# Kernel tuning notes

Measured on AMD Instinct MI355X. Metric: run time of the kernel, lower is better.

Reference implementation:

```python
import jax, jax.numpy as jnp
import numpy as np

B, H, O, M = 8192, 1024, 1024, 4

def setup_inputs() -> dict:
    key = jax.random.key(0)
    ks = jax.random.split(key, 8)
    state = jax.random.normal(ks[0], (B, H), dtype=jnp.float32)
    spectral_entropy = jax.random.uniform(ks[1], (B, 1), dtype=jnp.float32)
    curvature = jax.random.normal(ks[2], (B, 1), dtype=jnp.float32)
    # learned params
    modulation_basis = jax.random.normal(ks[3], (M, H, O), dtype=jnp.float32)
    gate_w = jax.random.normal(ks[4], (1, M), dtype=jnp.float32) / jnp.sqrt(1.0)
    gate_b = jax.random.normal(ks[5], (M,), dtype=jnp.float32) * 0.01
    prj_w = jax.random.normal(ks[6], (H, O), dtype=jnp.float32) / jnp.sqrt(H)
    prj_b = jax.random.normal(ks[7], (O,), dtype=jnp.float32) * 0.01
    return {"state": state, "spectral_entropy": spectral_entropy, "curvature": curvature,
            "modulation_basis": modulation_basis, "gate_w": gate_w, "gate_b": gate_b,
            "prj_w": prj_w, "prj_b": prj_b}

def reference(state, spectral_entropy, curvature, modulation_basis, gate_w, gate_b, prj_w, prj_b):
    # softmax gate over modes: [B, M]
    mod_weights = jax.nn.softmax(spectral_entropy @ gate_w + gate_b, axis=-1)
    # Algebraically fused form of einsum('bm,mho->bho') then einsum('bh,bho->bo'):
    # compute per-mode matvec results [B, M, O] (small), then mode-weighted sum.
    mode_out = jnp.einsum('bh,mho->bmo', state, modulation_basis)
    mischief_output = jnp.einsum('bm,bmo->bo', mod_weights, mode_out)
    base_output = state @ prj_w + prj_b
    mix = jax.nn.sigmoid(curvature)  # [B, 1]
    return (1.0 - mix) * base_output + mix * mischief_output
```

## Files before the change

kernel.cpp:

```cpp
#include <hip/hip_runtime.h>
#include <stdint.h>

typedef __attribute__((ext_vector_type(4))) float  float4v;
typedef __attribute__((ext_vector_type(8))) __bf16 bf16x8;
typedef __attribute__((ext_vector_type(8))) unsigned short ushort8;

#define B_DIM 8192
#define H_DIM 1024
#define O_DIM 1024

static __device__ __forceinline__ unsigned short f32_to_bf16(float f) {
  union { float f; unsigned int u; } v; v.f = f;
  unsigned int u = v.u;
  unsigned int r = u + 0x7FFFu + ((u >> 16) & 1u);
  return (unsigned short)(r >> 16);
}

__global__ void prep_inputs(const float* __restrict__ state,
                            const float* __restrict__ basis,
                            const float* __restrict__ prjw,
                            unsigned short* __restrict__ Abf,
                            unsigned short* __restrict__ Wt) {
  __shared__ __align__(16) unsigned short t[64 * 72];
  int bb = blockIdx.x;
  int tid = threadIdx.x;
  if (bb < 1280) {
    int m = bb >> 8, panel = bb & 255;
    int o0 = (panel & 15) * 64, h0 = (panel >> 4) * 64;
    const float* src = (m < 4) ? (basis + (size_t)m * H_DIM * O_DIM) : prjw;
    int r  = tid >> 4;
    int c4 = (tid & 15) * 4;
#pragma unroll
    for (int p = 0; p < 4; ++p) {
      int h = r + p * 16;
      float4v v = *(const float4v*)(src + (size_t)(h0 + h) * O_DIM + o0 + c4);
      t[(c4 + 0) * 72 + h] = f32_to_bf16(v.x);
      t[(c4 + 1) * 72 + h] = f32_to_bf16(v.y);
      t[(c4 + 2) * 72 + h] = f32_to_bf16(v.z);
      t[(c4 + 3) * 72 + h] = f32_to_bf16(v.w);
    }
    __syncthreads();
#pragma unroll
    for (int i = 0; i < 2; ++i) {
      int C = i * 256 + tid;
      int o = C >> 3, cc = C & 7;
      ushort8 val = *(const ushort8*)(t + o * 72 + cc * 8);
      *(ushort8*)(Wt + ((size_t)m * O_DIM + o0 + o) * H_DIM + h0 + cc * 8) = val;
    }
  } else {
    int i = (bb - 1280) * 256 + tid;
    float4v v0 = ((const float4v*)state)[i * 2];
    float4v v1 = ((const float4v*)state)[i * 2 + 1];
    ushort8 o;
    o[0] = f32_to_bf16(v0.x); o[1] = f32_to_bf16(v0.y);
    o[2] = f32_to_bf16(v0.z); o[3] = f32_to_bf16(v0.w);
    o[4] = f32_to_bf16(v1.x); o[5] = f32_to_bf16(v1.y);
    o[6] = f32_to_bf16(v1.z); o[7] = f32_to_bf16(v1.w);
    ((ushort8*)Abf)[i] = o;
  }
}

__global__ __launch_bounds__(512, 2)
void gemm_fused(const unsigned short* __restrict__ A,
                const unsigned short* __restrict__ Wt,
                const float* __restrict__ se, const float* __restrict__ curv,
                const float* __restrict__ gw, const float* __restrict__ gb,
                const float* __restrict__ prjb,
                float* __restrict__ out) {
  __shared__ __align__(16) unsigned char smem[115712];
  float* scf = (float*)(smem + 110592);

  const int tid  = threadIdx.x;
  const int lane = tid & 63;
  const int wave = tid >> 6;
  const int row0 = blockIdx.x * 256;
  const int col0 = blockIdx.y * 64;
  const int wrow = (wave >> 1) * 64;
  const int wcol = (wave & 1) * 32;
  const int q  = lane >> 4;
  const int ln = lane & 15;

  if (tid < 256) {
    int b = row0 + tid;
    float s = se[b];
    float l0 = fmaf(s, gw[0], gb[0]);
    float l1 = fmaf(s, gw[1], gb[1]);
    float l2 = fmaf(s, gw[2], gb[2]);
    float l3 = fmaf(s, gw[3], gb[3]);
    float mx = fmaxf(fmaxf(l0, l1), fmaxf(l2, l3));
    float e0 = __expf(l0 - mx), e1 = __expf(l1 - mx);
    float e2 = __expf(l2 - mx), e3 = __expf(l3 - mx);
    float mix = 1.0f / (1.0f + __expf(-curv[b]));
    float inv = mix / (e0 + e1 + e2 + e3);
    scf[0 * 256 + tid] = e0 * inv;
    scf[1 * 256 + tid] = e1 * inv;
    scf[2 * 256 + tid] = e2 * inv;
    scf[3 * 256 + tid] = e3 * inv;
    scf[4 * 256 + tid] = 1.0f - mix;
  }

  const unsigned short* gsrc[5];
  unsigned int ldsoff[5];
  if (wave < 4) {
#pragma unroll
    for (int j = 0; j < 4; ++j) {
      int c = wave * 4 + j;
      int row = c * 16 + (lane >> 2);
      int pos = lane & 3;
      int g = pos ^ ((row >> 1) & 3);
      gsrc[j] = A + (size_t)(row0 + row) * H_DIM + g * 8;
      ldsoff[j] = c * 1024;
    }
    gsrc[4] = gsrc[0]; ldsoff[4] = ldsoff[0];
  } else {
#pragma unroll
    for (int j = 0; j < 5; ++j) {
      int c = (wave - 4) * 5 + j;
      int m = c >> 2;
      int r = (c & 3) * 16 + (lane >> 2);
      int pos = lane & 3;
      int g = pos ^ ((r >> 1) & 3);
      gsrc[j] = Wt + (size_t)m * O_DIM * H_DIM + (size_t)(col0 + r) * H_DIM + g * 8;
      ldsoff[j] = 16384 + c * 1024;
    }
  }

  float4v acc[5][4][2];
#pragma unroll
  for (int m = 0; m < 5; ++m)
#pragma unroll
    for (int i = 0; i < 4; ++i)
#pragma unroll
      for (int j = 0; j < 2; ++j)
        acc[m][i][j] = (float4v){0.f, 0.f, 0.f, 0.f};

#define ISSUE_STAGE(koff, boff)                                                 \
  do {                                                                          \
    if (wave < 4) {                                                             \
      _Pragma("unroll")                                                         \
      for (int _j = 0; _j < 4; ++_j)                                            \
        __builtin_amdgcn_global_load_lds(                                       \
            (const __attribute__((address_space(1))) void*)(gsrc[_j] + (koff)), \
            (__attribute__((address_space(3))) void*)(smem + (boff) + ldsoff[_j]),\
            16, 0, 0);                                                          \
    } else {                                                                    \
      _Pragma("unroll")                                                         \
      for (int _j = 0; _j < 5; ++_j)                                            \
        __builtin_amdgcn_global_load_lds(                                       \
            (const __attribute__((address_space(1))) void*)(gsrc[_j] + (koff)), \
            (__attribute__((address_space(3))) void*)(smem + (boff) + ldsoff[_j]),\
            16, 0, 0);                                                          \
    }                                                                           \
  } while (0)

#define WAITV_STEADY                                                            \
  do {                                                                          \
    if (wave < 4) asm volatile("s_waitcnt vmcnt(8)" ::: "memory");              \
    else          asm volatile("s_waitcnt vmcnt(10)" ::: "memory");             \
  } while (0)
#define WAITV_ONE                                                               \
  do {                                                                          \
    if (wave < 4) asm volatile("s_waitcnt vmcnt(4)" ::: "memory");              \
    else          asm volatile("s_waitcnt vmcnt(5)" ::: "memory");              \
  } while (0)
#define WAITV_ZERO asm volatile("s_waitcnt vmcnt(0)" ::: "memory")

#define COMPUTE_STAGE(boff)                                                     \
  do {                                                                          \
    const unsigned short* _sA = (const unsigned short*)(smem + (boff));         \
    const unsigned short* _sB = _sA + 8192;                                     \
    __builtin_amdgcn_s_setprio(1);                                              \
    bf16x8 _af[4];                                                              \
    _Pragma("unroll")                                                           \
    for (int _t = 0; _t < 4; ++_t) {                                            \
      int _ra = wrow + _t * 16 + ln;                                            \
      int _ps = q ^ ((_ra >> 1) & 3);                                           \
      _af[_t] = *(const bf16x8*)(_sA + _ra * 32 + _ps * 8);                     \
    }                                                                           \
    _Pragma("unroll")                                                           \
    for (int _m = 0; _m < 5; ++_m) {                                            \
      bf16x8 _b0, _b1;                                                          \
      {                                                                         \
        int _rb = wcol + ln;                                                    \
        int _p0 = q ^ ((_rb >> 1) & 3);                                         \
        _b0 = *(const bf16x8*)(_sB + _m * 2048 + _rb * 32 + _p0 * 8);           \
        int _r1 = wcol + 16 + ln;                                               \
        int _p1 = q ^ ((_r1 >> 1) & 3);                                         \
        _b1 = *(const bf16x8*)(_sB + _m * 2048 + _r1 * 32 + _p1 * 8);           \
      }                                                                         \
      _Pragma("unroll")                                                         \
      for (int _ti = 0; _ti < 4; ++_ti) {                                       \
        acc[_m][_ti][0] = __builtin_amdgcn_mfma_f32_16x16x32_bf16(              \
            _af[_ti], _b0, acc[_m][_ti][0], 0, 0, 0);                           \
        acc[_m][_ti][1] = __builtin_amdgcn_mfma_f32_16x16x32_bf16(              \
            _af[_ti], _b1, acc[_m][_ti][1], 0, 0, 0);                           \
      }                                                                         \
    }                                                                           \
    __builtin_amdgcn_s_setprio(0);                                              \
  } while (0)

  ISSUE_STAGE(0, 0u);
  ISSUE_STAGE(32, 36864u);
  ISSUE_STAGE(64, 73728u);
  asm volatile("s_waitcnt lgkmcnt(0)" ::: "memory");
  WAITV_STEADY;
  __builtin_amdgcn_s_barrier();

  unsigned int boff = 0u;
  int kk = 96;
  for (int s = 0; s < 29; ++s) {
    COMPUTE_STAGE(boff);
    __builtin_amdgcn_s_barrier();
    ISSUE_STAGE(kk, boff);
    WAITV_STEADY;
    __builtin_amdgcn_s_barrier();
    kk += 32;
    boff = (boff == 73728u) ? 0u : boff + 36864u;
  }
  COMPUTE_STAGE(boff);
  WAITV_ONE;
  __builtin_amdgcn_s_barrier();
  boff = (boff == 73728u) ? 0u : boff + 36864u;
  COMPUTE_STAGE(boff);
  WAITV_ZERO;
  __builtin_amdgcn_s_barrier();
  boff = (boff == 73728u) ? 0u : boff + 36864u;
  COMPUTE_STAGE(boff);

  __syncthreads();
  float* fbuf = (float*)smem;
#pragma unroll
  for (int ti = 0; ti < 4; ++ti) {
    int rl = wrow + ti * 16 + q * 4;
#pragma unroll
    for (int tj = 0; tj < 2; ++tj) {
      int cc = wcol + tj * 16 + ln;
#pragma unroll
      for (int r = 0; r < 4; ++r) {
        float v = 0.f;
#pragma unroll
        for (int m = 0; m < 5; ++m)
          v += scf[m * 256 + rl + r] * acc[m][ti][tj][r];
        fbuf[(rl + r) * 68 + cc] = v;
      }
    }
  }
  __syncthreads();
#pragma unroll
  for (int i = 0; i < 8; ++i) {
    int L = i * 512 + tid;
    int row = L >> 4, c4 = L & 15;
    float4v v = *(const float4v*)(fbuf + row * 68 + c4 * 4);
    float cb = scf[4 * 256 + row];
    float4v pb = *(const float4v*)(prjb + col0 + c4 * 4);
    v += cb * pb;
    *(float4v*)(out + (size_t)(row0 + row) * O_DIM + col0 + c4 * 4) = v;
  }
#undef ISSUE_STAGE
#undef WAITV_STEADY
#undef WAITV_ONE
#undef WAITV_ZERO
#undef COMPUTE_STAGE
}

extern "C" void kernel_launch(void* const* d_in, const int* in_sizes, int n_in,
                              void* d_out, int out_size, void* d_ws, size_t ws_size,
                              hipStream_t stream) {
  const float* state = (const float*)d_in[0];
  const float* se    = (const float*)d_in[1];
  const float* curv  = (const float*)d_in[2];
  const float* basis = (const float*)d_in[3];
  const float* gw    = (const float*)d_in[4];
  const float* gb    = (const float*)d_in[5];
  const float* prjw  = (const float*)d_in[6];
  const float* prjb  = (const float*)d_in[7];
  float* out = (float*)d_out;

  char* ws = (char*)d_ws;
  unsigned short* Abf = (unsigned short*)ws;
  unsigned short* Wt  = (unsigned short*)(ws + (size_t)16 * 1024 * 1024);

  prep_inputs<<<5376, 256, 0, stream>>>(state, basis, prjw, Abf, Wt);
  dim3 gg(B_DIM / 256, O_DIM / 64);
  gemm_fused<<<gg, 512, 0, stream>>>(Abf, Wt, se, curv, gw, gb, prjb, out);
}
```

Before: 180.6 us.

## Switch to four-slot LDS ring with loads interleaved into per-mode MFMA phases

Grows the LDS staging ring from three to four slots, so the next global-to-LDS copy can target a free slot while the current one is still being read. That copy is now split across the first three mode phases of each K step, each phase bracketed by barriers and a raised-priority MFMA burst. It also precomputes the swizzled LDS fragment offsets and advances the global pointers incrementally. The aim is to hide memory latency behind MFMA work and drop the separate issue and barrier step that followed each compute stage. The cost is many more workgroup barriers per K step and a larger LDS footprint.

```diff
diff --git a/kernel.cpp b/kernel.cpp
--- a/kernel.cpp
+++ b/kernel.cpp
@@ -67,8 +67,8 @@
                 const float* __restrict__ gw, const float* __restrict__ gb,
                 const float* __restrict__ prjb,
                 float* __restrict__ out) {
-  __shared__ __align__(16) unsigned char smem[115712];
-  float* scf = (float*)(smem + 110592);
+  __shared__ __align__(16) unsigned char smem[152576];
+  float* scf = (float*)(smem + 147456);
 
   const int tid  = threadIdx.x;
   const int lane = tid & 63;
@@ -80,6 +80,140 @@
   const int q  = lane >> 4;
   const int ln = lane & 15;
 
+  const unsigned short* gsrc[5];
+  unsigned int ldsoff[5];
+  if (wave < 4) {
+#pragma unroll
+    for (int j = 0; j < 4; ++j) {
+      int c = wave * 4 + j;
+      int row = c * 16 + (lane >> 2);
+      int pos = lane & 3;
+      int g = pos ^ ((row >> 1) & 3);
+      gsrc[j] = A + (size_t)(row0 + row) * H_DIM + g * 8;
+      ldsoff[j] = c * 1024;
+    }
+    gsrc[4] = gsrc[0]; ldsoff[4] = ldsoff[0];
+  } else {
+#pragma unroll
+    for (int j = 0; j < 5; ++j) {
+      int c = (wave - 4) * 5 + j;
+      int m = c >> 2;
+      int r = (c & 3) * 16 + (lane >> 2);
+      int pos = lane & 3;
+      int g = pos ^ ((r >> 1) & 3);
+      gsrc[j] = Wt + (size_t)m * O_DIM * H_DIM + (size_t)(col0 + r) * H_DIM + g * 8;
+      ldsoff[j] = 16384 + c * 1024;
+    }
+  }
+
+  int aoffs[4];
+#pragma unroll
+  for (int t = 0; t < 4; ++t) {
+    int ra = wrow + t * 16 + ln;
+    aoffs[t] = ra * 32 + (q ^ ((ra >> 1) & 3)) * 8;
+  }
+  int boffs[2];
+  {
+    int rb = wcol + ln;      boffs[0] = rb * 32 + (q ^ ((rb >> 1) & 3)) * 8;
+    int r1 = wcol + 16 + ln; boffs[1] = r1 * 32 + (q ^ ((r1 >> 1) & 3)) * 8;
+  }
+
+  float4v acc[5][4][2];
+#pragma unroll
+  for (int m = 0; m < 5; ++m)
+#pragma unroll
+    for (int i = 0; i < 4; ++i)
+#pragma unroll
+      for (int j = 0; j < 2; ++j)
+        acc[m][i][j] = (float4v){0.f, 0.f, 0.f, 0.f};
+
+#define GLDS(j_)                                                                \
+  __builtin_amdgcn_global_load_lds(                                             \
+      (const __attribute__((address_space(1))) void*)(gsrc[j_]),                \
+      (__attribute__((address_space(3))) void*)(dst + ldsoff[j_]), 16, 0, 0)
+
+#define ISSUE_HALF(slot)                                                        \
+  do {                                                                          \
+    unsigned char* dst = smem + (slot) * 36864;                                 \
+    GLDS(0); GLDS(1); GLDS(2); GLDS(3);                                         \
+    if (wave >= 4) GLDS(4);                                                     \
+    _Pragma("unroll") for (int _j = 0; _j < 5; ++_j) gsrc[_j] += 32;            \
+  } while (0)
+
+#define GUARD_2L                                                                \
+  do { if (wave < 4) asm volatile("s_waitcnt vmcnt(8)" ::: "memory");           \
+       else          asm volatile("s_waitcnt vmcnt(10)" ::: "memory"); } while (0)
+#define GUARD_1L                                                                \
+  do { if (wave < 4) asm volatile("s_waitcnt vmcnt(4)" ::: "memory");           \
+       else          asm volatile("s_waitcnt vmcnt(5)" ::: "memory"); } while (0)
+#define GUARD_0   asm volatile("s_waitcnt vmcnt(0)" ::: "memory")
+#define GUARD_NONE do { } while (0)
+
+#define MFMA8(m_)                                                               \
+  do {                                                                          \
+    acc[m_][0][0] = __builtin_amdgcn_mfma_f32_16x16x32_bf16(af0, b0, acc[m_][0][0], 0, 0, 0); \
+    acc[m_][1][0] = __builtin_amdgcn_mfma_f32_16x16x32_bf16(af1, b0, acc[m_][1][0], 0, 0, 0); \
+    acc[m_][2][0] = __builtin_amdgcn_mfma_f32_16x16x32_bf16(af2, b0, acc[m_][2][0], 0, 0, 0); \
+    acc[m_][3][0] = __builtin_amdgcn_mfma_f32_16x16x32_bf16(af3, b0, acc[m_][3][0], 0, 0, 0); \
+    acc[m_][0][1] = __builtin_amdgcn_mfma_f32_16x16x32_bf16(af0, b1, acc[m_][0][1], 0, 0, 0); \
+    acc[m_][1][1] = __builtin_amdgcn_mfma_f32_16x16x32_bf16(af1, b1, acc[m_][1][1], 0, 0, 0); \
+    acc[m_][2][1] = __builtin_amdgcn_mfma_f32_16x16x32_bf16(af2, b1, acc[m_][2][1], 0, 0, 0); \
+    acc[m_][3][1] = __builtin_amdgcn_mfma_f32_16x16x32_bf16(af3, b1, acc[m_][3][1], 0, 0, 0); \
+  } while (0)
+
+#define PH_BAR_MFMA(m_)                                                         \
+  do {                                                                          \
+    __builtin_amdgcn_s_barrier();                                               \
+    asm volatile("s_waitcnt lgkmcnt(0)" ::: "memory");                          \
+    __builtin_amdgcn_s_setprio(1);                                              \
+    MFMA8(m_);                                                                  \
+    __builtin_amdgcn_s_setprio(0);                                              \
+  } while (0)
+
+#define HALF_TILE(hh, DO_GLDS, GUARD)                                           \
+  do {                                                                          \
+    const unsigned short* sA = (const unsigned short*)(smem + ((hh) & 3) * 36864);\
+    const unsigned short* sB = sA + 8192;                                       \
+    unsigned char* dst = smem + (((hh) + 3) & 3) * 36864; (void)dst;            \
+                                        \
+    bf16x8 af0 = *(const bf16x8*)(sA + aoffs[0]);                               \
+    bf16x8 af1 = *(const bf16x8*)(sA + aoffs[1]);                               \
+    bf16x8 af2 = *(const bf16x8*)(sA + aoffs[2]);                               \
+    bf16x8 af3 = *(const bf16x8*)(sA + aoffs[3]);                               \
+    bf16x8 b0 = *(const bf16x8*)(sB + boffs[0]);                                \
+    bf16x8 b1 = *(const bf16x8*)(sB + boffs[1]);                                \
+    if (DO_GLDS) { GLDS(0); GLDS(1); }                                          \
+    PH_BAR_MFMA(0);                                                             \
+    __builtin_amdgcn_s_barrier();                                               \
+                                                  \
+    b0 = *(const bf16x8*)(sB + 2048 + boffs[0]);                                \
+    b1 = *(const bf16x8*)(sB + 2048 + boffs[1]);                                \
+    if (DO_GLDS) { GLDS(2); GLDS(3); }                                          \
+    PH_BAR_MFMA(1);                                                             \
+    __builtin_amdgcn_s_barrier();                                               \
+                                \
+    b0 = *(const bf16x8*)(sB + 4096 + boffs[0]);                                \
+    b1 = *(const bf16x8*)(sB + 4096 + boffs[1]);                                \
+    if (DO_GLDS) {                                                              \
+      if (wave >= 4) GLDS(4);                                                   \
+      _Pragma("unroll") for (int _j = 0; _j < 5; ++_j) gsrc[_j] += 32;          \
+    }                                                                           \
+    PH_BAR_MFMA(2);                                                             \
+    __builtin_amdgcn_s_barrier();                                               \
+                                                          \
+    b0 = *(const bf16x8*)(sB + 6144 + boffs[0]);                                \
+    b1 = *(const bf16x8*)(sB + 6144 + boffs[1]);                                \
+    PH_BAR_MFMA(3);                                                             \
+    __builtin_amdgcn_s_barrier();                                               \
+                   \
+    b0 = *(const bf16x8*)(sB + 8192 + boffs[0]);                                \
+    b1 = *(const bf16x8*)(sB + 8192 + boffs[1]);                                \
+    PH_BAR_MFMA(4);                                                             \
+    GUARD;                                                                      \
+    __builtin_amdgcn_s_barrier();                                               \
+  } while (0)
+
+  ISSUE_HALF(0); ISSUE_HALF(1); ISSUE_HALF(2);
   if (tid < 256) {
     int b = row0 + tid;
     float s = se[b];
@@ -98,134 +232,20 @@
     scf[3 * 256 + tid] = e3 * inv;
     scf[4 * 256 + tid] = 1.0f - mix;
   }
-
-  const unsigned short* gsrc[5];
-  unsigned int ldsoff[5];
-  if (wave < 4) {
-#pragma unroll
-    for (int j = 0; j < 4; ++j) {
-      int c = wave * 4 + j;
-      int row = c * 16 + (lane >> 2);
-      int pos = lane & 3;
-      int g = pos ^ ((row >> 1) & 3);
-      gsrc[j] = A + (size_t)(row0 + row) * H_DIM + g * 8;
-      ldsoff[j] = c * 1024;
-    }
-    gsrc[4] = gsrc[0]; ldsoff[4] = ldsoff[0];
-  } else {
-#pragma unroll
-    for (int j = 0; j < 5; ++j) {
-      int c = (wave - 4) * 5 + j;
-      int m = c >> 2;
-      int r = (c & 3) * 16 + (lane >> 2);
-      int pos = lane & 3;
-      int g = pos ^ ((r >> 1) & 3);
-      gsrc[j] = Wt + (size_t)m * O_DIM * H_DIM + (size_t)(col0 + r) * H_DIM + g * 8;
-      ldsoff[j] = 16384 + c * 1024;
-    }
-  }
-
-  float4v acc[5][4][2];
-#pragma unroll
-  for (int m = 0; m < 5; ++m)
-#pragma unroll
-    for (int i = 0; i < 4; ++i)
-#pragma unroll
-      for (int j = 0; j < 2; ++j)
-        acc[m][i][j] = (float4v){0.f, 0.f, 0.f, 0.f};
-
-#define ISSUE_STAGE(koff, boff)                                                 \
-  do {                                                                          \
-    if (wave < 4) {                                                             \
-      _Pragma("unroll")                                                         \
-      for (int _j = 0; _j < 4; ++_j)                                            \
-        __builtin_amdgcn_global_load_lds(                                       \
-            (const __attribute__((address_space(1))) void*)(gsrc[_j] + (koff)), \
-            (__attribute__((address_space(3))) void*)(smem + (boff) + ldsoff[_j]),\
-            16, 0, 0);                                                          \
-    } else {                                                                    \
-      _Pragma("unroll")                                                         \
-      for (int _j = 0; _j < 5; ++_j)                                            \
-        __builtin_amdgcn_global_load_lds(                                       \
-            (const __attribute__((address_space(1))) void*)(gsrc[_j] + (koff)), \
-            (__attribute__((address_space(3))) void*)(smem + (boff) + ldsoff[_j]),\
-            16, 0, 0);                                                          \
-    }                                                                           \
-  } while (0)
-
-#define WAITV_STEADY                                                            \
-  do {                                                                          \
-    if (wave < 4) asm volatile("s_waitcnt vmcnt(8)" ::: "memory");              \
-    else          asm volatile("s_waitcnt vmcnt(10)" ::: "memory");             \
-  } while (0)
-#define WAITV_ONE                                                               \
-  do {                                                                          \
-    if (wave < 4) asm volatile("s_waitcnt vmcnt(4)" ::: "memory");              \
-    else          asm volatile("s_waitcnt vmcnt(5)" ::: "memory");              \
-  } while (0)
-#define WAITV_ZERO asm volatile("s_waitcnt vmcnt(0)" ::: "memory")
-
-#define COMPUTE_STAGE(boff)                                                     \
-  do {                                                                          \
-    const unsigned short* _sA = (const unsigned short*)(smem + (boff));         \
-    const unsigned short* _sB = _sA + 8192;                                     \
-    __builtin_amdgcn_s_setprio(1);                                              \
-    bf16x8 _af[4];                                                              \
-    _Pragma("unroll")                                                           \
-    for (int _t = 0; _t < 4; ++_t) {                                            \
-      int _ra = wrow + _t * 16 + ln;                                            \
-      int _ps = q ^ ((_ra >> 1) & 3);                                           \
-      _af[_t] = *(const bf16x8*)(_sA + _ra * 32 + _ps * 8);                     \
-    }                                                                           \
-    _Pragma("unroll")                                                           \
-    for (int _m = 0; _m < 5; ++_m) {                                            \
-      bf16x8 _b0, _b1;                                                          \
-      {                                                                         \
-        int _rb = wcol + ln;                                                    \
-        int _p0 = q ^ ((_rb >> 1) & 3);                                         \
-        _b0 = *(const bf16x8*)(_sB + _m * 2048 + _rb * 32 + _p0 * 8);           \
-        int _r1 = wcol + 16 + ln;                                               \
-        int _p1 = q ^ ((_r1 >> 1) & 3);                                         \
-        _b1 = *(const bf16x8*)(_sB + _m * 2048 + _r1 * 32 + _p1 * 8);           \
-      }                                                                         \
-      _Pragma("unroll")                                                         \
-      for (int _ti = 0; _ti < 4; ++_ti) {                                       \
-        acc[_m][_ti][0] = __builtin_amdgcn_mfma_f32_16x16x32_bf16(              \
-            _af[_ti], _b0, acc[_m][_ti][0], 0, 0, 0);                           \
-        acc[_m][_ti][1] = __builtin_amdgcn_mfma_f32_16x16x32_bf16(              \
-            _af[_ti], _b1, acc[_m][_ti][1], 0, 0, 0);                           \
-      }                                                                         \
-    }                                                                           \
-    __builtin_amdgcn_s_setprio(0);                                              \
-  } while (0)
-
-  ISSUE_STAGE(0, 0u);
-  ISSUE_STAGE(32, 36864u);
-  ISSUE_STAGE(64, 73728u);
   asm volatile("s_waitcnt lgkmcnt(0)" ::: "memory");
-  WAITV_STEADY;
+  GUARD_2L;
   __builtin_amdgcn_s_barrier();
 
-  unsigned int boff = 0u;
-  int kk = 96;
-  for (int s = 0; s < 29; ++s) {
-    COMPUTE_STAGE(boff);
-    __builtin_amdgcn_s_barrier();
-    ISSUE_STAGE(kk, boff);
-    WAITV_STEADY;
-    __builtin_amdgcn_s_barrier();
-    kk += 32;
-    boff = (boff == 73728u) ? 0u : boff + 36864u;
-  }
-  COMPUTE_STAGE(boff);
-  WAITV_ONE;
-  __builtin_amdgcn_s_barrier();
-  boff = (boff == 73728u) ? 0u : boff + 36864u;
-  COMPUTE_STAGE(boff);
-  WAITV_ZERO;
-  __builtin_amdgcn_s_barrier();
-  boff = (boff == 73728u) ? 0u : boff + 36864u;
-  COMPUTE_STAGE(boff);
+  for (int h = 0; h < 28; h += 4) {
+    HALF_TILE(h + 0, true, GUARD_2L);
+    HALF_TILE(h + 1, true, GUARD_2L);
+    HALF_TILE(h + 2, true, GUARD_2L);
+    HALF_TILE(h + 3, true, GUARD_2L);
+  }
+  HALF_TILE(28, true,  GUARD_2L);
+  HALF_TILE(29, false, GUARD_1L);
+  HALF_TILE(30, false, GUARD_0);
+  HALF_TILE(31, false, GUARD_NONE);
 
   __syncthreads();
   float* fbuf = (float*)smem;
@@ -256,11 +276,15 @@
     v += cb * pb;
     *(float4v*)(out + (size_t)(row0 + row) * O_DIM + col0 + c4 * 4) = v;
   }
-#undef ISSUE_STAGE
-#undef WAITV_STEADY
-#undef WAITV_ONE
-#undef WAITV_ZERO
-#undef COMPUTE_STAGE
+#undef GLDS
+#undef ISSUE_HALF
+#undef GUARD_2L
+#undef GUARD_1L
+#undef GUARD_0
+#undef GUARD_NONE
+#undef MFMA8
+#undef PH_BAR_MFMA
+#undef HALF_TILE
 }
 
 extern "C" void kernel_launch(void* const* d_in, const int* in_sizes, int n_in,
```

New measurement: 281.0 us. +55.6%, slower.

## Restructure GEMM main loop: one barrier per stage, prefetch fragments across barrier

Applied to the files above, without the earlier changes.

The K-loop is rewritten from two barriers per stage to a single barrier. The next stage's global-to-LDS copy is issued before computing, and the A and mode-0/1 B fragments for the following stage are read right after the barrier, so the LDS reads overlap the wait. Pointer increments and precomputed LDS offsets replace per-stage address math. Only two stages are prefetched before the gate softmax setup, which moves behind the first issues. This cuts synchronization and exposed LDS latency, at the cost of a shallower in-flight prefetch depth and more register pressure from the extra live fragments.

```diff
diff --git a/kernel.cpp b/kernel.cpp
--- a/kernel.cpp
+++ b/kernel.cpp
@@ -80,6 +80,129 @@
   const int q  = lane >> 4;
   const int ln = lane & 15;
 
+  const unsigned short* gsrc[5];
+  unsigned int ldsoff[5];
+  if (wave < 4) {
+#pragma unroll
+    for (int j = 0; j < 4; ++j) {
+      int c = wave * 4 + j;
+      int row = c * 16 + (lane >> 2);
+      int pos = lane & 3;
+      int g = pos ^ ((row >> 1) & 3);
+      gsrc[j] = A + (size_t)(row0 + row) * H_DIM + g * 8;
+      ldsoff[j] = c * 1024;
+    }
+    gsrc[4] = gsrc[0]; ldsoff[4] = ldsoff[0];
+  } else {
+#pragma unroll
+    for (int j = 0; j < 5; ++j) {
+      int c = (wave - 4) * 5 + j;
+      int m = c >> 2;
+      int r = (c & 3) * 16 + (lane >> 2);
+      int pos = lane & 3;
+      int g = pos ^ ((r >> 1) & 3);
+      gsrc[j] = Wt + (size_t)m * O_DIM * H_DIM + (size_t)(col0 + r) * H_DIM + g * 8;
+      ldsoff[j] = 16384 + c * 1024;
+    }
+  }
+
+  int aoffs[4];
+#pragma unroll
+  for (int t = 0; t < 4; ++t) {
+    int ra = wrow + t * 16 + ln;
+    aoffs[t] = ra * 32 + (q ^ ((ra >> 1) & 3)) * 8;
+  }
+  int boffs[2];
+  {
+    int rb = wcol + ln;      boffs[0] = rb * 32 + (q ^ ((rb >> 1) & 3)) * 8;
+    int r1 = wcol + 16 + ln; boffs[1] = r1 * 32 + (q ^ ((r1 >> 1) & 3)) * 8;
+  }
+
+  float4v acc[5][4][2];
+#pragma unroll
+  for (int m = 0; m < 5; ++m)
+#pragma unroll
+    for (int i = 0; i < 4; ++i)
+#pragma unroll
+      for (int j = 0; j < 2; ++j)
+        acc[m][i][j] = (float4v){0.f, 0.f, 0.f, 0.f};
+
+#define ISSUE_SLOT(boff_)                                                       \
+  do {                                                                          \
+    unsigned char* _dst = smem + (boff_);                                       \
+    __builtin_amdgcn_global_load_lds(                                           \
+        (const __attribute__((address_space(1))) void*)gsrc[0],                 \
+        (__attribute__((address_space(3))) void*)(_dst + ldsoff[0]), 16, 0, 0); \
+    __builtin_amdgcn_global_load_lds(                                           \
+        (const __attribute__((address_space(1))) void*)gsrc[1],                 \
+        (__attribute__((address_space(3))) void*)(_dst + ldsoff[1]), 16, 0, 0); \
+    __builtin_amdgcn_global_load_lds(                                           \
+        (const __attribute__((address_space(1))) void*)gsrc[2],                 \
+        (__attribute__((address_space(3))) void*)(_dst + ldsoff[2]), 16, 0, 0); \
+    __builtin_amdgcn_global_load_lds(                                           \
+        (const __attribute__((address_space(1))) void*)gsrc[3],                 \
+        (__attribute__((address_space(3))) void*)(_dst + ldsoff[3]), 16, 0, 0); \
+    if (wave >= 4)                                                              \
+      __builtin_amdgcn_global_load_lds(                                         \
+          (const __attribute__((address_space(1))) void*)gsrc[4],               \
+          (__attribute__((address_space(3))) void*)(_dst + ldsoff[4]), 16, 0, 0);\
+    _Pragma("unroll") for (int _j = 0; _j < 5; ++_j) gsrc[_j] += 32;            \
+  } while (0)
+
+#define WAITL                                                                   \
+  do { if (wave < 4) asm volatile("s_waitcnt vmcnt(4)" ::: "memory");           \
+       else          asm volatile("s_waitcnt vmcnt(5)" ::: "memory"); } while (0)
+
+  bf16x8 a0, a1, a2, a3, b00, b01, b10, b11;
+
+#define READ_PH0(boff_)                                                         \
+  do {                                                                          \
+    const unsigned short* _sA = (const unsigned short*)(smem + (boff_));        \
+    const unsigned short* _sB = _sA + 8192;                                     \
+    a0 = *(const bf16x8*)(_sA + aoffs[0]);                                      \
+    a1 = *(const bf16x8*)(_sA + aoffs[1]);                                      \
+    a2 = *(const bf16x8*)(_sA + aoffs[2]);                                      \
+    a3 = *(const bf16x8*)(_sA + aoffs[3]);                                      \
+    b00 = *(const bf16x8*)(_sB + boffs[0]);                                     \
+    b01 = *(const bf16x8*)(_sB + boffs[1]);                                     \
+    b10 = *(const bf16x8*)(_sB + 2048 + boffs[0]);                              \
+    b11 = *(const bf16x8*)(_sB + 2048 + boffs[1]);                              \
+  } while (0)
+
+#define MFMA_MODE(m_, bb0, bb1)                                                 \
+  do {                                                                          \
+    acc[m_][0][0] = __builtin_amdgcn_mfma_f32_16x16x32_bf16(a0, bb0, acc[m_][0][0], 0, 0, 0); \
+    acc[m_][1][0] = __builtin_amdgcn_mfma_f32_16x16x32_bf16(a1, bb0, acc[m_][1][0], 0, 0, 0); \
+    acc[m_][2][0] = __builtin_amdgcn_mfma_f32_16x16x32_bf16(a2, bb0, acc[m_][2][0], 0, 0, 0); \
+    acc[m_][3][0] = __builtin_amdgcn_mfma_f32_16x16x32_bf16(a3, bb0, acc[m_][3][0], 0, 0, 0); \
+    acc[m_][0][1] = __builtin_amdgcn_mfma_f32_16x16x32_bf16(a0, bb1, acc[m_][0][1], 0, 0, 0); \
+    acc[m_][1][1] = __builtin_amdgcn_mfma_f32_16x16x32_bf16(a1, bb1, acc[m_][1][1], 0, 0, 0); \
+    acc[m_][2][1] = __builtin_amdgcn_mfma_f32_16x16x32_bf16(a2, bb1, acc[m_][2][1], 0, 0, 0); \
+    acc[m_][3][1] = __builtin_amdgcn_mfma_f32_16x16x32_bf16(a3, bb1, acc[m_][3][1], 0, 0, 0); \
+  } while (0)
+
+#define PH1_READS(boff_)                                                        \
+  const unsigned short* _cB = (const unsigned short*)(smem + (boff_)) + 8192;   \
+  bf16x8 c20 = *(const bf16x8*)(_cB + 2 * 2048 + boffs[0]);                     \
+  bf16x8 c21 = *(const bf16x8*)(_cB + 2 * 2048 + boffs[1]);                     \
+  bf16x8 c30 = *(const bf16x8*)(_cB + 3 * 2048 + boffs[0]);                     \
+  bf16x8 c31 = *(const bf16x8*)(_cB + 3 * 2048 + boffs[1]);                     \
+  bf16x8 c40 = *(const bf16x8*)(_cB + 4 * 2048 + boffs[0]);                     \
+  bf16x8 c41 = *(const bf16x8*)(_cB + 4 * 2048 + boffs[1])
+
+#define MFMA_ALL5                                                               \
+  do {                                                                          \
+    __builtin_amdgcn_s_setprio(1);                                              \
+    MFMA_MODE(0, b00, b01);                                                     \
+    MFMA_MODE(1, b10, b11);                                                     \
+    MFMA_MODE(2, c20, c21);                                                     \
+    MFMA_MODE(3, c30, c31);                                                     \
+    MFMA_MODE(4, c40, c41);                                                     \
+    __builtin_amdgcn_s_setprio(0);                                              \
+  } while (0)
+
+  ISSUE_SLOT(0u);
+  ISSUE_SLOT(36864u);
   if (tid < 256) {
     int b = row0 + tid;
     float s = se[b];
@@ -98,134 +221,35 @@
     scf[3 * 256 + tid] = e3 * inv;
     scf[4 * 256 + tid] = 1.0f - mix;
   }
-
-  const unsigned short* gsrc[5];
-  unsigned int ldsoff[5];
-  if (wave < 4) {
-#pragma unroll
-    for (int j = 0; j < 4; ++j) {
-      int c = wave * 4 + j;
-      int row = c * 16 + (lane >> 2);
-      int pos = lane & 3;
-      int g = pos ^ ((row >> 1) & 3);
-      gsrc[j] = A + (size_t)(row0 + row) * H_DIM + g * 8;
-      ldsoff[j] = c * 1024;
-    }
-    gsrc[4] = gsrc[0]; ldsoff[4] = ldsoff[0];
-  } else {
-#pragma unroll
-    for (int j = 0; j < 5; ++j) {
-      int c = (wave - 4) * 5 + j;
-      int m = c >> 2;
-      int r = (c & 3) * 16 + (lane >> 2);
-      int pos = lane & 3;
-      int g = pos ^ ((r >> 1) & 3);
-      gsrc[j] = Wt + (size_t)m * O_DIM * H_DIM + (size_t)(col0 + r) * H_DIM + g * 8;
-      ldsoff[j] = 16384 + c * 1024;
-    }
-  }
-
-  float4v acc[5][4][2];
-#pragma unroll
-  for (int m = 0; m < 5; ++m)
-#pragma unroll
-    for (int i = 0; i < 4; ++i)
-#pragma unroll
-      for (int j = 0; j < 2; ++j)
-        acc[m][i][j] = (float4v){0.f, 0.f, 0.f, 0.f};
-
-#define ISSUE_STAGE(koff, boff)                                                 \
-  do {                                                                          \
-    if (wave < 4) {                                                             \
-      _Pragma("unroll")                                                         \
-      for (int _j = 0; _j < 4; ++_j)                                            \
-        __builtin_amdgcn_global_load_lds(                                       \
-            (const __attribute__((address_space(1))) void*)(gsrc[_j] + (koff)), \
-            (__attribute__((address_space(3))) void*)(smem + (boff) + ldsoff[_j]),\
-            16, 0, 0);                                                          \
-    } else {                                                                    \
-      _Pragma("unroll")                                                         \
-      for (int _j = 0; _j < 5; ++_j)                                            \
-        __builtin_amdgcn_global_load_lds(                                       \
-            (const __attribute__((address_space(1))) void*)(gsrc[_j] + (koff)), \
-            (__attribute__((address_space(3))) void*)(smem + (boff) + ldsoff[_j]),\
-            16, 0, 0);                                                          \
-    }                                                                           \
-  } while (0)
-
-#define WAITV_STEADY                                                            \
-  do {                                                                          \
-    if (wave < 4) asm volatile("s_waitcnt vmcnt(8)" ::: "memory");              \
-    else          asm volatile("s_waitcnt vmcnt(10)" ::: "memory");             \
-  } while (0)
-#define WAITV_ONE                                                               \
-  do {                                                                          \
-    if (wave < 4) asm volatile("s_waitcnt vmcnt(4)" ::: "memory");              \
-    else          asm volatile("s_waitcnt vmcnt(5)" ::: "memory");              \
-  } while (0)
-#define WAITV_ZERO asm volatile("s_waitcnt vmcnt(0)" ::: "memory")
-
-#define COMPUTE_STAGE(boff)                                                     \
-  do {                                                                          \
-    const unsigned short* _sA = (const unsigned short*)(smem + (boff));         \
-    const unsigned short* _sB = _sA + 8192;                                     \
-    __builtin_amdgcn_s_setprio(1);                                              \
-    bf16x8 _af[4];                                                              \
-    _Pragma("unroll")                                                           \
-    for (int _t = 0; _t < 4; ++_t) {                                            \
-      int _ra = wrow + _t * 16 + ln;                                            \
-      int _ps = q ^ ((_ra >> 1) & 3);                                           \
-      _af[_t] = *(const bf16x8*)(_sA + _ra * 32 + _ps * 8);                     \
-    }                                                                           \
-    _Pragma("unroll")                                                           \
-    for (int _m = 0; _m < 5; ++_m) {                                            \
-      bf16x8 _b0, _b1;                                                          \
-      {                                                                         \
-        int _rb = wcol + ln;                                                    \
-        int _p0 = q ^ ((_rb >> 1) & 3);                                         \
-        _b0 = *(const bf16x8*)(_sB + _m * 2048 + _rb * 32 + _p0 * 8);           \
-        int _r1 = wcol + 16 + ln;                                               \
-        int _p1 = q ^ ((_r1 >> 1) & 3);                                         \
-        _b1 = *(const bf16x8*)(_sB + _m * 2048 + _r1 * 32 + _p1 * 8);           \
-      }                                                                         \
-      _Pragma("unroll")                                                         \
-      for (int _ti = 0; _ti < 4; ++_ti) {                                       \
-        acc[_m][_ti][0] = __builtin_amdgcn_mfma_f32_16x16x32_bf16(              \
-            _af[_ti], _b0, acc[_m][_ti][0], 0, 0, 0);                           \
-        acc[_m][_ti][1] = __builtin_amdgcn_mfma_f32_16x16x32_bf16(              \
-            _af[_ti], _b1, acc[_m][_ti][1], 0, 0, 0);                           \
-      }                                                                         \
-    }                                                                           \
-    __builtin_amdgcn_s_setprio(0);                                              \
-  } while (0)
-
-  ISSUE_STAGE(0, 0u);
-  ISSUE_STAGE(32, 36864u);
-  ISSUE_STAGE(64, 73728u);
-  asm volatile("s_waitcnt lgkmcnt(0)" ::: "memory");
-  WAITV_STEADY;
+  WAITL;
   __builtin_amdgcn_s_barrier();
-
-  unsigned int boff = 0u;
-  int kk = 96;
-  for (int s = 0; s < 29; ++s) {
-    COMPUTE_STAGE(boff);
+  __builtin_amdgcn_sched_barrier(0);
+  READ_PH0(0u);
+
+  unsigned int cS = 0u, nS = 36864u, iS = 73728u;
+#pragma unroll 1
+  for (int s = 0; s < 30; ++s) {
+    ISSUE_SLOT(iS);
+    PH1_READS(cS);
+    MFMA_ALL5;
+    WAITL;
     __builtin_amdgcn_s_barrier();
-    ISSUE_STAGE(kk, boff);
-    WAITV_STEADY;
+    __builtin_amdgcn_sched_barrier(0);
+    READ_PH0(nS);
+    unsigned int t_ = cS; cS = nS; nS = iS; iS = t_;
+  }
+  {
+    PH1_READS(cS);
+    MFMA_ALL5;
+    asm volatile("s_waitcnt vmcnt(0)" ::: "memory");
     __builtin_amdgcn_s_barrier();
-    kk += 32;
-    boff = (boff == 73728u) ? 0u : boff + 36864u;
-  }
-  COMPUTE_STAGE(boff);
-  WAITV_ONE;
-  __builtin_amdgcn_s_barrier();
-  boff = (boff == 73728u) ? 0u : boff + 36864u;
-  COMPUTE_STAGE(boff);
-  WAITV_ZERO;
-  __builtin_amdgcn_s_barrier();
-  boff = (boff == 73728u) ? 0u : boff + 36864u;
-  COMPUTE_STAGE(boff);
+    __builtin_amdgcn_sched_barrier(0);
+    READ_PH0(nS);
+  }
+  {
+    PH1_READS(nS);
+    MFMA_ALL5;
+  }
 
   __syncthreads();
   float* fbuf = (float*)smem;
@@ -256,11 +280,12 @@
     v += cb * pb;
     *(float4v*)(out + (size_t)(row0 + row) * O_DIM + col0 + c4 * 4) = v;
   }
-#undef ISSUE_STAGE
-#undef WAITV_STEADY
-#undef WAITV_ONE
-#undef WAITV_ZERO
-#undef COMPUTE_STAGE
+#undef ISSUE_SLOT
+#undef WAITL
+#undef READ_PH0
+#undef MFMA_MODE
+#undef PH1_READS
+#undef MFMA_ALL5
 }
 
 extern "C" void kernel_launch(void* const* d_in, const int* in_sizes, int n_in,
```

Measured after the change: 183.0 us. Within noise of the previous version (+1.3%).
